# Performance work log

Measured on AMD Instinct MI355X. Metric: run time of the kernel, lower is better.

Reference implementation:

```python
import jax, jax.numpy as jnp
import numpy as np


def setup_inputs() -> dict:
    key = jax.random.key(0)
    k1, k2 = jax.random.split(key)
    x = jax.random.normal(k1, (32, 64, 64, 64), dtype=jnp.float32)
    codebook = jax.random.normal(k2, (1024, 64), dtype=jnp.float32)
    return {"x": x, "codebook": codebook}


def reference(x, codebook):
    # x: (B, D, H, W)  codebook: (K, D)
    B, D = x.shape[0], x.shape[1]
    spatial = x.shape[2:]
    flat = x.reshape(B, D, -1).transpose(0, 2, 1)  # (B, N, D)
    dot = jnp.einsum("bnd,kd->bnk", flat, codebook)
    cb_norm = jnp.sum(codebook * codebook, axis=-1)  # (K,)
    indices = jnp.argmin(cb_norm[None, None, :] - 2.0 * dot, axis=-1)  # (B, N)
    quantized = codebook[indices]  # (B, N, D) gather
    out = quantized.transpose(0, 2, 1).reshape(x.shape)
    return out, indices.reshape((B,) + spatial)
```

## Files before the change

### kernel.cpp

```cpp
#include <hip/hip_runtime.h>


typedef _Float16 f16x8 __attribute__((ext_vector_type(8)));
typedef float    f32x4 __attribute__((ext_vector_type(4)));

#define VQ_D    64
#define VQ_HW   4096
#define VQ_NPOS 131072
#define SC      2048.0f
#define EPS_Q   16
#define WS_CBN  65536
#define WS_CBT  66560
#define WS_CNT  132096
#define WS_LIST 132100

__global__ __launch_bounds__(256)
void vq_prep(const float* __restrict__ cb, float* __restrict__ ws)
{
    const int tid = threadIdx.x;
    const int blk = blockIdx.x;
    if (blk < 64) {
        const int it   = blk * 256 + tid;
        const int ct   = it >> 8;
        const int s    = (it >> 6) & 3;
        const int lane = it & 63;
        const int ks   = s & 1, isR = s >> 1;
        const int n    = ct * 16 + (lane & 15);
        const int k0   = ks * 32 + (lane >> 4) * 8;
        const float* src = cb + n * 64 + k0;
        f16x8 o;
        #pragma unroll
        for (int j = 0; j < 8; ++j) {
            const float b = src[j];
            const _Float16 bh = (_Float16)b;
            o[j] = isR ? (_Float16)((b - (float)bh) * (-2.0f * SC))
                       : (_Float16)(-2.0f * (float)bh);
        }
        ((f16x8*)ws)[it] = o;
    } else if (blk < 128) {
        const int it = (blk - 64) * 256 + tid;
        const int k = it >> 4, j4 = it & 15;
        ((float4*)(ws + WS_CBT))[j4 * 1024 + k] = ((const float4*)cb)[it];
    } else {
        const int k = (blk - 128) * 256 + tid;
        const float4* row = (const float4*)(cb + k * 64);
        float a0 = 0.f, a1 = 0.f, a2 = 0.f, a3 = 0.f;
        #pragma unroll
        for (int j = 0; j < 16; ++j) {
            const float4 c = row[j];
            a0 = fmaf(c.x, c.x, a0); a1 = fmaf(c.y, c.y, a1);
            a2 = fmaf(c.z, c.z, a2); a3 = fmaf(c.w, c.w, a3);
        }
        ws[WS_CBN + k] = (a0 + a1) + (a2 + a3);
        if (k == 0) ((int*)ws)[WS_CNT] = 0;
    }
}

#define GLOAD_LDS(GP, LP)                                                     \
    __builtin_amdgcn_global_load_lds(                                         \
        (const __attribute__((address_space(1))) unsigned int*)(GP),          \
        (__attribute__((address_space(3))) unsigned int*)(LP), 16, 0, 0)

__global__ __launch_bounds__(256, 4)
void vq_main(const float* __restrict__ x,
             const float* __restrict__ cb,
             float* __restrict__ ws,
             float* __restrict__ out,
             float* __restrict__ idx_out)
{
    __shared__ f16x8 bbuf[2][1024];
    __shared__ float cn_lds[1024];
    __shared__ int   sk[128];
    __shared__ int   smg[128];

    const int tid  = threadIdx.x;
    const int lane = tid & 63;
    const int wv   = tid >> 6;
    const int m    = lane & 15;
    const int q    = lane >> 4;

    const int p0 = blockIdx.x * 128;
    const int b  = p0 >> 12;
    const int n0 = p0 & (VQ_HW - 1);
    const float* xw = x + (size_t)b * (VQ_D * VQ_HW) + n0 + wv * 32;

    ((float4*)cn_lds)[tid] = ((const float4*)(ws + WS_CBN))[tid];

    {
        const char* gsrc = (const char*)ws + wv * 4096 + lane * 16;
        char*       ldst = (char*)&bbuf[0][0] + wv * 4096;
        GLOAD_LDS(gsrc, ldst);                GLOAD_LDS(gsrc + 1024, ldst + 1024);
        GLOAD_LDS(gsrc + 2048, ldst + 2048);  GLOAD_LDS(gsrc + 3072, ldst + 3072);
    }

    f16x8 Ah[2][2], Ra[2][2];
    #pragma unroll
    for (int tl = 0; tl < 2; ++tl)
        #pragma unroll
        for (int ks = 0; ks < 2; ++ks) {
            f16x8 h8, r8;
            #pragma unroll
            for (int j = 0; j < 8; ++j) {
                const float v = xw[(size_t)(ks * 32 + q * 8 + j) * VQ_HW + tl * 16 + m];
                const _Float16 vh = (_Float16)v;
                h8[j] = vh;
                r8[j] = (_Float16)((v - (float)vh) * SC);
            }
            Ah[tl][ks] = h8; Ra[tl][ks] = r8;
        }

    int d1[2][4], d2[2][4];
    #pragma unroll
    for (int tl = 0; tl < 2; ++tl)
        #pragma unroll
        for (int r = 0; r < 4; ++r) { d1[tl][r] = 0x7FFFFFFF; d2[tl][r] = 0x7FFFFFFF; }

    const f32x4 zero4 = {0.f, 0.f, 0.f, 0.f};

    for (int cc = 0; cc < 16; ++cc) {
        __syncthreads();
        if (cc < 15) {
            const char* gsrc = (const char*)ws + (size_t)(cc + 1) * 16384 + wv * 4096 + lane * 16;
            char*       ldst = (char*)&bbuf[(cc + 1) & 1][0] + wv * 4096;
            GLOAD_LDS(gsrc, ldst);                GLOAD_LDS(gsrc + 1024, ldst + 1024);
            GLOAD_LDS(gsrc + 2048, ldst + 2048);  GLOAD_LDS(gsrc + 3072, ldst + 3072);
        }
        const f16x8* bufc = &bbuf[cc & 1][0];
        #pragma unroll
        for (int ctl = 0; ctl < 4; ++ctl) {
            const int ctg = cc * 4 + ctl;
            const f16x8 B0 = bufc[ctl * 256 +       lane];
            const f16x8 B1 = bufc[ctl * 256 +  64 + lane];
            const f16x8 R0 = bufc[ctl * 256 + 128 + lane];
            const f16x8 R1 = bufc[ctl * 256 + 192 + lane];
            const float cv = cn_lds[ctg * 16 + m];
            const f32x4 Ci = {cv, cv, cv, cv};
            f32x4 acm[2], acc[2];
            #pragma unroll
            for (int tl = 0; tl < 2; ++tl) {
                acm[tl] = __builtin_amdgcn_mfma_f32_16x16x32_f16(Ah[tl][0], B0, Ci,      0,0,0);
                acm[tl] = __builtin_amdgcn_mfma_f32_16x16x32_f16(Ah[tl][1], B1, acm[tl], 0,0,0);
                acc[tl] = __builtin_amdgcn_mfma_f32_16x16x32_f16(Ah[tl][0], R0, zero4,   0,0,0);
                acc[tl] = __builtin_amdgcn_mfma_f32_16x16x32_f16(Ah[tl][1], R1, acc[tl], 0,0,0);
                acc[tl] = __builtin_amdgcn_mfma_f32_16x16x32_f16(Ra[tl][0], B0, acc[tl], 0,0,0);
                acc[tl] = __builtin_amdgcn_mfma_f32_16x16x32_f16(Ra[tl][1], B1, acc[tl], 0,0,0);
            }
            const int code_ = ctg * 16 + m;
            #pragma unroll
            for (int tl = 0; tl < 2; ++tl)
                #pragma unroll
                for (int r = 0; r < 4; ++r) {
                    const float qf  = fmaf(acm[tl][r], SC, acc[tl][r]);
                    const int   key = ((int)qf << 10) | code_;
                    const int   t   = (key > d1[tl][r]) ? key : d1[tl][r];
                    d2[tl][r] = (t < d2[tl][r]) ? t : d2[tl][r];
                    d1[tl][r] = (key < d1[tl][r]) ? key : d1[tl][r];
                }
        }
    }

    #pragma unroll
    for (int off = 1; off < 16; off <<= 1)
        #pragma unroll
        for (int tl = 0; tl < 2; ++tl)
            #pragma unroll
            for (int r = 0; r < 4; ++r) {
                const int od1 = __shfl_xor(d1[tl][r], off, 64);
                const int od2 = __shfl_xor(d2[tl][r], off, 64);
                const int mx  = (d1[tl][r] > od1) ? d1[tl][r] : od1;
                const int mn2 = (d2[tl][r] < od2) ? d2[tl][r] : od2;
                d2[tl][r] = (mx < mn2) ? mx : mn2;
                d1[tl][r] = (d1[tl][r] < od1) ? d1[tl][r] : od1;
            }

    if (m == 0) {
        #pragma unroll
        for (int tl = 0; tl < 2; ++tl)
            #pragma unroll
            for (int r = 0; r < 4; ++r) {
                const int li = wv * 32 + tl * 16 + q * 4 + r;
                sk[li]  = d1[tl][r] & 1023;
                smg[li] = (d2[tl][r] >> 10) - (d1[tl][r] >> 10);
            }
    }
    __syncthreads();

    const int pos  = tid & 127;
    const int half = tid >> 7;
    const int bk   = sk[pos];
    if (half == 0) {
        idx_out[p0 + pos] = (float)bk;
        if (smg[pos] < EPS_Q) {
            const int slot = atomicAdd((int*)ws + WS_CNT, 1);
            ((int*)ws)[WS_LIST + slot] = p0 + pos;
        }
    }
    const float4* cr = (const float4*)(cb + (size_t)bk * VQ_D) + half * 8;
    float* ob = out + (size_t)b * (VQ_D * VQ_HW) + (size_t)(half * 32) * VQ_HW + n0 + pos;
    #pragma unroll
    for (int d4 = 0; d4 < 8; ++d4) {
        const float4 v = cr[d4];
        ob[(size_t)(d4 * 4 + 0) * VQ_HW] = v.x;
        ob[(size_t)(d4 * 4 + 1) * VQ_HW] = v.y;
        ob[(size_t)(d4 * 4 + 2) * VQ_HW] = v.z;
        ob[(size_t)(d4 * 4 + 3) * VQ_HW] = v.w;
    }
}

__global__ __launch_bounds__(64)
void vq_rescan(const float* __restrict__ x,
               const float* __restrict__ cb,
               const float* __restrict__ ws,
               float* __restrict__ out,
               float* __restrict__ idx_out)
{
    __shared__ float xs[VQ_D];
    const int lane = threadIdx.x;
    const int cnt  = ((const int*)ws)[WS_CNT];
    const int* list = (const int*)ws + WS_LIST;
    const float*  cnb  = ws + WS_CBN;
    const float4* cbT4 = (const float4*)(ws + WS_CBT);

    for (int i = blockIdx.x; i < cnt; i += gridDim.x) {
        const int p = list[i];
        const int b = p >> 12, n = p & (VQ_HW - 1);
        xs[lane] = x[(size_t)b * (VQ_D * VQ_HW) + (size_t)lane * VQ_HW + n];
        __syncthreads();
        float4 xr[16];
        #pragma unroll
        for (int j = 0; j < 16; ++j) xr[j] = ((const float4*)xs)[j];

        float bd = 3.4e38f; int bk = 0;
        #pragma unroll 4
        for (int t = 0; t < 16; ++t) {
            const int code = t * 64 + lane;
            float a0 = 0.f, a1 = 0.f, a2 = 0.f, a3 = 0.f;
            #pragma unroll
            for (int j4 = 0; j4 < 16; ++j4) {
                const float4 c = cbT4[j4 * 1024 + code];
                a0 = fmaf(xr[j4].x, c.x, a0); a1 = fmaf(xr[j4].y, c.y, a1);
                a2 = fmaf(xr[j4].z, c.z, a2); a3 = fmaf(xr[j4].w, c.w, a3);
            }
            const float dist = fmaf(-2.0f, (a0 + a1) + (a2 + a3), cnb[code]);
            if (dist < bd) { bd = dist; bk = code; }
        }
        #pragma unroll
        for (int off = 1; off < 64; off <<= 1) {
            const float od = __shfl_xor(bd, off, 64);
            const int   ok = __shfl_xor(bk, off, 64);
            if (od < bd || (od == bd && ok < bk)) { bd = od; bk = ok; }
        }
        out[(size_t)b * (VQ_D * VQ_HW) + (size_t)lane * VQ_HW + n] = cb[(size_t)bk * VQ_D + lane];
        if (lane == 0) idx_out[p] = (float)bk;
        __syncthreads();
    }
}

extern "C" void kernel_launch(void* const* d_in, const int* in_sizes, int n_in,
                              void* d_out, int out_size, void* d_ws, size_t ws_size,
                              hipStream_t stream) {
    const float* x  = (const float*)d_in[0];
    const float* cb = (const float*)d_in[1];
    float* out = (float*)d_out;
    float* idx = out + (size_t)VQ_NPOS * VQ_D;
    float* ws  = (float*)d_ws;

    vq_prep  <<<dim3(132),  dim3(256), 0, stream>>>(cb, ws);
    vq_main  <<<dim3(1024), dim3(256), 0, stream>>>(x, cb, ws, out, idx);
    vq_rescan<<<dim3(1024), dim3(64),  0, stream>>>(x, cb, ws, out, idx);
}
```

Before: 159.7 us.

## Halve positions per block, interleave codebook norms into chunks, raise occupancy

Each wave now handles 16 positions instead of 32, so blocks cover 64 positions and the grid doubles to 2048 blocks. The launch bound is raised from 4 to 8 blocks per SM. The prep kernel writes the codebook in chunks of two code tiles with their norms interleaved, so norms arrive through the same global-to-LDS pipeline and the separate norm table in shared memory goes away. This cuts registers and shared memory per block to raise occupancy, but each block now streams the whole codebook through LDS for half as many positions. That doubles codebook traffic and the number of barriers per unit of work.

```diff
diff --git a/kernel.cpp b/kernel.cpp
--- a/kernel.cpp
+++ b/kernel.cpp
@@ -9,10 +9,11 @@
 #define VQ_NPOS 131072
 #define SC      2048.0f
 #define EPS_Q   16
-#define WS_CBN  65536
-#define WS_CBT  66560
-#define WS_CNT  132096
-#define WS_LIST 132100
+#define CHB     9216
+#define WS_CBN  73728
+#define WS_CBT  74752
+#define WS_CNT  140288
+#define WS_LIST 140292
 
 __global__ __launch_bounds__(256)
 void vq_prep(const float* __restrict__ cb, float* __restrict__ ws)
@@ -36,7 +37,8 @@
             o[j] = isR ? (_Float16)((b - (float)bh) * (-2.0f * SC))
                        : (_Float16)(-2.0f * (float)bh);
         }
-        ((f16x8*)ws)[it] = o;
+        *(f16x8*)((char*)ws + (size_t)(ct >> 1) * CHB + (ct & 1) * 4096
+                            + s * 1024 + lane * 16) = o;
     } else if (blk < 128) {
         const int it = (blk - 64) * 256 + tid;
         const int k = it >> 4, j4 = it & 15;
@@ -51,7 +53,11 @@
             a0 = fmaf(c.x, c.x, a0); a1 = fmaf(c.y, c.y, a1);
             a2 = fmaf(c.z, c.z, a2); a3 = fmaf(c.w, c.w, a3);
         }
-        ws[WS_CBN + k] = (a0 + a1) + (a2 + a3);
+        const float cn = (a0 + a1) + (a2 + a3);
+        ws[WS_CBN + k] = cn;
+        const int ct = k >> 4, i = k & 15;
+        *(float*)((char*)ws + (size_t)(ct >> 1) * CHB + 8192
+                            + (ct & 1) * 64 + i * 4) = cn;
         if (k == 0) ((int*)ws)[WS_CNT] = 0;
     }
 }
@@ -61,17 +67,16 @@
         (const __attribute__((address_space(1))) unsigned int*)(GP),          \
         (__attribute__((address_space(3))) unsigned int*)(LP), 16, 0, 0)
 
-__global__ __launch_bounds__(256, 4)
+__global__ __launch_bounds__(256, 8)
 void vq_main(const float* __restrict__ x,
              const float* __restrict__ cb,
              float* __restrict__ ws,
              float* __restrict__ out,
              float* __restrict__ idx_out)
 {
-    __shared__ f16x8 bbuf[2][1024];
-    __shared__ float cn_lds[1024];
-    __shared__ int   sk[128];
-    __shared__ int   smg[128];
+    __shared__ f16x8 bbuf[2][CHB / 16];
+    __shared__ int   sk[64];
+    __shared__ int   smg[64];
 
     const int tid  = threadIdx.x;
     const int lane = tid & 63;
@@ -79,126 +84,109 @@
     const int m    = lane & 15;
     const int q    = lane >> 4;
 
-    const int p0 = blockIdx.x * 128;
+    const int p0 = blockIdx.x * 64;
     const int b  = p0 >> 12;
     const int n0 = p0 & (VQ_HW - 1);
-    const float* xw = x + (size_t)b * (VQ_D * VQ_HW) + n0 + wv * 32;
-
-    ((float4*)cn_lds)[tid] = ((const float4*)(ws + WS_CBN))[tid];
+    const float* xw = x + (size_t)b * (VQ_D * VQ_HW) + n0 + wv * 16;
 
     {
-        const char* gsrc = (const char*)ws + wv * 4096 + lane * 16;
-        char*       ldst = (char*)&bbuf[0][0] + wv * 4096;
-        GLOAD_LDS(gsrc, ldst);                GLOAD_LDS(gsrc + 1024, ldst + 1024);
-        GLOAD_LDS(gsrc + 2048, ldst + 2048);  GLOAD_LDS(gsrc + 3072, ldst + 3072);
-    }
-
-    f16x8 Ah[2][2], Ra[2][2];
-    #pragma unroll
-    for (int tl = 0; tl < 2; ++tl)
-        #pragma unroll
-        for (int ks = 0; ks < 2; ++ks) {
-            f16x8 h8, r8;
-            #pragma unroll
-            for (int j = 0; j < 8; ++j) {
-                const float v = xw[(size_t)(ks * 32 + q * 8 + j) * VQ_HW + tl * 16 + m];
-                const _Float16 vh = (_Float16)v;
-                h8[j] = vh;
-                r8[j] = (_Float16)((v - (float)vh) * SC);
-            }
-            Ah[tl][ks] = h8; Ra[tl][ks] = r8;
-        }
-
-    int d1[2][4], d2[2][4];
-    #pragma unroll
-    for (int tl = 0; tl < 2; ++tl)
-        #pragma unroll
-        for (int r = 0; r < 4; ++r) { d1[tl][r] = 0x7FFFFFFF; d2[tl][r] = 0x7FFFFFFF; }
+        const char* gs = (const char*)ws + lane * 16;
+        char*       ld = (char*)&bbuf[0][0];
+        for (int o = wv; o < 9; o += 4) GLOAD_LDS(gs + o * 1024, ld + o * 1024);
+    }
+
+    f16x8 Ah[2], Ra[2];
+    #pragma unroll
+    for (int ks = 0; ks < 2; ++ks) {
+        f16x8 h8, r8;
+        #pragma unroll
+        for (int j = 0; j < 8; ++j) {
+            const float v = xw[(size_t)(ks * 32 + q * 8 + j) * VQ_HW + m];
+            const _Float16 vh = (_Float16)v;
+            h8[j] = vh;
+            r8[j] = (_Float16)((v - (float)vh) * SC);
+        }
+        Ah[ks] = h8; Ra[ks] = r8;
+    }
+
+    int d1[4], d2[4];
+    #pragma unroll
+    for (int r = 0; r < 4; ++r) { d1[r] = 0x7FFFFFFF; d2[r] = 0x7FFFFFFF; }
 
     const f32x4 zero4 = {0.f, 0.f, 0.f, 0.f};
 
-    for (int cc = 0; cc < 16; ++cc) {
+    for (int cc = 0; cc < 32; ++cc) {
         __syncthreads();
-        if (cc < 15) {
-            const char* gsrc = (const char*)ws + (size_t)(cc + 1) * 16384 + wv * 4096 + lane * 16;
-            char*       ldst = (char*)&bbuf[(cc + 1) & 1][0] + wv * 4096;
-            GLOAD_LDS(gsrc, ldst);                GLOAD_LDS(gsrc + 1024, ldst + 1024);
-            GLOAD_LDS(gsrc + 2048, ldst + 2048);  GLOAD_LDS(gsrc + 3072, ldst + 3072);
-        }
-        const f16x8* bufc = &bbuf[cc & 1][0];
-        #pragma unroll
-        for (int ctl = 0; ctl < 4; ++ctl) {
-            const int ctg = cc * 4 + ctl;
-            const f16x8 B0 = bufc[ctl * 256 +       lane];
-            const f16x8 B1 = bufc[ctl * 256 +  64 + lane];
-            const f16x8 R0 = bufc[ctl * 256 + 128 + lane];
-            const f16x8 R1 = bufc[ctl * 256 + 192 + lane];
-            const float cv = cn_lds[ctg * 16 + m];
+        if (cc < 31) {
+            const char* gs = (const char*)ws + (size_t)(cc + 1) * CHB + lane * 16;
+            char*       ld = (char*)&bbuf[(cc + 1) & 1][0];
+            for (int o = wv; o < 9; o += 4) GLOAD_LDS(gs + o * 1024, ld + o * 1024);
+        }
+        const char* bufc = (const char*)&bbuf[cc & 1][0];
+        #pragma unroll
+        for (int ci = 0; ci < 2; ++ci) {
+            const int ctg = cc * 2 + ci;
+            const f16x8* bp = (const f16x8*)(bufc + ci * 4096);
+            const f16x8 R0 = bp[128 + lane];
+            const f16x8 R1 = bp[192 + lane];
+            f32x4 acc = __builtin_amdgcn_mfma_f32_16x16x32_f16(Ah[0], R0, zero4, 0,0,0);
+            acc       = __builtin_amdgcn_mfma_f32_16x16x32_f16(Ah[1], R1, acc,   0,0,0);
+            const f16x8 B0 = bp[lane];
+            const f16x8 B1 = bp[64 + lane];
+            acc       = __builtin_amdgcn_mfma_f32_16x16x32_f16(Ra[0], B0, acc,   0,0,0);
+            acc       = __builtin_amdgcn_mfma_f32_16x16x32_f16(Ra[1], B1, acc,   0,0,0);
+            const float cv = *(const float*)(bufc + 8192 + ci * 64 + m * 4);
             const f32x4 Ci = {cv, cv, cv, cv};
-            f32x4 acm[2], acc[2];
-            #pragma unroll
-            for (int tl = 0; tl < 2; ++tl) {
-                acm[tl] = __builtin_amdgcn_mfma_f32_16x16x32_f16(Ah[tl][0], B0, Ci,      0,0,0);
-                acm[tl] = __builtin_amdgcn_mfma_f32_16x16x32_f16(Ah[tl][1], B1, acm[tl], 0,0,0);
-                acc[tl] = __builtin_amdgcn_mfma_f32_16x16x32_f16(Ah[tl][0], R0, zero4,   0,0,0);
-                acc[tl] = __builtin_amdgcn_mfma_f32_16x16x32_f16(Ah[tl][1], R1, acc[tl], 0,0,0);
-                acc[tl] = __builtin_amdgcn_mfma_f32_16x16x32_f16(Ra[tl][0], B0, acc[tl], 0,0,0);
-                acc[tl] = __builtin_amdgcn_mfma_f32_16x16x32_f16(Ra[tl][1], B1, acc[tl], 0,0,0);
-            }
+            f32x4 acm = __builtin_amdgcn_mfma_f32_16x16x32_f16(Ah[0], B0, Ci,  0,0,0);
+            acm       = __builtin_amdgcn_mfma_f32_16x16x32_f16(Ah[1], B1, acm, 0,0,0);
             const int code_ = ctg * 16 + m;
             #pragma unroll
-            for (int tl = 0; tl < 2; ++tl)
-                #pragma unroll
-                for (int r = 0; r < 4; ++r) {
-                    const float qf  = fmaf(acm[tl][r], SC, acc[tl][r]);
-                    const int   key = ((int)qf << 10) | code_;
-                    const int   t   = (key > d1[tl][r]) ? key : d1[tl][r];
-                    d2[tl][r] = (t < d2[tl][r]) ? t : d2[tl][r];
-                    d1[tl][r] = (key < d1[tl][r]) ? key : d1[tl][r];
-                }
+            for (int r = 0; r < 4; ++r) {
+                const float qf  = fmaf(acm[r], SC, acc[r]);
+                const int   key = ((int)qf << 10) | code_;
+                const int   t   = (key > d1[r]) ? key : d1[r];
+                d2[r] = (t < d2[r]) ? t : d2[r];
+                d1[r] = (key < d1[r]) ? key : d1[r];
+            }
         }
     }
 
     #pragma unroll
     for (int off = 1; off < 16; off <<= 1)
         #pragma unroll
-        for (int tl = 0; tl < 2; ++tl)
-            #pragma unroll
-            for (int r = 0; r < 4; ++r) {
-                const int od1 = __shfl_xor(d1[tl][r], off, 64);
-                const int od2 = __shfl_xor(d2[tl][r], off, 64);
-                const int mx  = (d1[tl][r] > od1) ? d1[tl][r] : od1;
-                const int mn2 = (d2[tl][r] < od2) ? d2[tl][r] : od2;
-                d2[tl][r] = (mx < mn2) ? mx : mn2;
-                d1[tl][r] = (d1[tl][r] < od1) ? d1[tl][r] : od1;
-            }
+        for (int r = 0; r < 4; ++r) {
+            const int od1 = __shfl_xor(d1[r], off, 64);
+            const int od2 = __shfl_xor(d2[r], off, 64);
+            const int mx  = (d1[r] > od1) ? d1[r] : od1;
+            const int mn2 = (d2[r] < od2) ? d2[r] : od2;
+            d2[r] = (mx < mn2) ? mx : mn2;
+            d1[r] = (d1[r] < od1) ? d1[r] : od1;
+        }
 
     if (m == 0) {
         #pragma unroll
-        for (int tl = 0; tl < 2; ++tl)
-            #pragma unroll
-            for (int r = 0; r < 4; ++r) {
-                const int li = wv * 32 + tl * 16 + q * 4 + r;
-                sk[li]  = d1[tl][r] & 1023;
-                smg[li] = (d2[tl][r] >> 10) - (d1[tl][r] >> 10);
-            }
+        for (int r = 0; r < 4; ++r) {
+            const int li = wv * 16 + q * 4 + r;
+            sk[li]  = d1[r] & 1023;
+            smg[li] = (d2[r] >> 10) - (d1[r] >> 10);
+        }
     }
     __syncthreads();
 
-    const int pos  = tid & 127;
-    const int half = tid >> 7;
+    const int pos  = tid & 63;
+    const int part = tid >> 6;
     const int bk   = sk[pos];
-    if (half == 0) {
+    if (part == 0) {
         idx_out[p0 + pos] = (float)bk;
         if (smg[pos] < EPS_Q) {
             const int slot = atomicAdd((int*)ws + WS_CNT, 1);
             ((int*)ws)[WS_LIST + slot] = p0 + pos;
         }
     }
-    const float4* cr = (const float4*)(cb + (size_t)bk * VQ_D) + half * 8;
-    float* ob = out + (size_t)b * (VQ_D * VQ_HW) + (size_t)(half * 32) * VQ_HW + n0 + pos;
-    #pragma unroll
-    for (int d4 = 0; d4 < 8; ++d4) {
+    const float4* cr = (const float4*)(cb + (size_t)bk * VQ_D) + part * 4;
+    float* ob = out + (size_t)b * (VQ_D * VQ_HW) + (size_t)(part * 16) * VQ_HW + n0 + pos;
+    #pragma unroll
+    for (int d4 = 0; d4 < 4; ++d4) {
         const float4 v = cr[d4];
         ob[(size_t)(d4 * 4 + 0) * VQ_HW] = v.x;
         ob[(size_t)(d4 * 4 + 1) * VQ_HW] = v.y;
@@ -266,6 +254,6 @@
     float* ws  = (float*)d_ws;
 
     vq_prep  <<<dim3(132),  dim3(256), 0, stream>>>(cb, ws);
-    vq_main  <<<dim3(1024), dim3(256), 0, stream>>>(x, cb, ws, out, idx);
+    vq_main  <<<dim3(2048), dim3(256), 0, stream>>>(x, cb, ws, out, idx);
     vq_rescan<<<dim3(1024), dim3(64),  0, stream>>>(x, cb, ws, out, idx);
 }
```

After: 172.8 us. +8.2%, slower.

## Fold scaled codebook norms into chunked workspace and single accumulator MFMA chain

Applied to the files above, without the earlier changes.

The workspace is re-laid out into chunks that carry each block of codebook tiles together with its pre-scaled norms. The main loop stages one chunk per half-iteration with manual double buffering, which removes the separate norm LDS array. The high and low distance accumulators are merged into one MFMA chain by pre-scaling the fp16 high part of x by 2048 and seeding the accumulator with the scaled norm. This drops the per-element fma and the zero-init chain. The top-2 update uses v_med3_i32 in place of max/min sequences. It adds an extra register set (Ak) and changes the rounding behaviour, so EPS_Q is widened to 20 to cover the added error.

```diff
diff --git a/kernel.cpp b/kernel.cpp
--- a/kernel.cpp
+++ b/kernel.cpp
@@ -8,11 +8,13 @@
 #define VQ_HW   4096
 #define VQ_NPOS 131072
 #define SC      2048.0f
-#define EPS_Q   16
-#define WS_CBN  65536
-#define WS_CBT  66560
-#define WS_CNT  132096
-#define WS_LIST 132100
+#define EPS_Q   20
+#define CHB     16640
+#define CHBP    17664
+#define WS_CBN  66560
+#define WS_CBT  67584
+#define WS_CNT  133120
+#define WS_LIST 133124
 
 __global__ __launch_bounds__(256)
 void vq_prep(const float* __restrict__ cb, float* __restrict__ ws)
@@ -36,7 +38,8 @@
             o[j] = isR ? (_Float16)((b - (float)bh) * (-2.0f * SC))
                        : (_Float16)(-2.0f * (float)bh);
         }
-        ((f16x8*)ws)[it] = o;
+        *(f16x8*)((char*)ws + (size_t)(ct >> 2) * CHB + (ct & 3) * 4096
+                            + s * 1024 + lane * 16) = o;
     } else if (blk < 128) {
         const int it = (blk - 64) * 256 + tid;
         const int k = it >> 4, j4 = it & 15;
@@ -51,7 +54,11 @@
             a0 = fmaf(c.x, c.x, a0); a1 = fmaf(c.y, c.y, a1);
             a2 = fmaf(c.z, c.z, a2); a3 = fmaf(c.w, c.w, a3);
         }
-        ws[WS_CBN + k] = (a0 + a1) + (a2 + a3);
+        const float cn = (a0 + a1) + (a2 + a3);
+        ws[WS_CBN + k] = cn;
+        const int ct = k >> 4, i = k & 15;
+        *(float*)((char*)ws + (size_t)(ct >> 2) * CHB + 16384
+                            + (ct & 3) * 64 + i * 4) = cn * 2048.0f;
         if (k == 0) ((int*)ws)[WS_CNT] = 0;
     }
 }
@@ -60,6 +67,56 @@
     __builtin_amdgcn_global_load_lds(                                         \
         (const __attribute__((address_space(1))) unsigned int*)(GP),          \
         (__attribute__((address_space(3))) unsigned int*)(LP), 16, 0, 0)
+
+#define STAGE(GS, BOFF)                                                       \
+    {                                                                         \
+        char* ld_ = (char*)bbuf + (BOFF) + wv * 1024;                         \
+        const char* gs_ = (GS) + wv * 1024;                                   \
+        GLOAD_LDS(gs_,         ld_);                                          \
+        GLOAD_LDS(gs_ + 4096,  ld_ + 4096);                                   \
+        GLOAD_LDS(gs_ + 8192,  ld_ + 8192);                                   \
+        GLOAD_LDS(gs_ + 12288, ld_ + 12288);                                  \
+        if (wv == 0 && lane < 16)                                             \
+            GLOAD_LDS((GS) + 16384, (char*)bbuf + (BOFF) + 16384);            \
+    }
+
+#define CT_BODY(BOFF, SLOT, CTG)                                              \
+    {                                                                         \
+        const f16x8 B0 = *(const f16x8*)(lp + (BOFF) + (SLOT) * 4096);        \
+        const f16x8 B1 = *(const f16x8*)(lp + (BOFF) + (SLOT) * 4096 + 1024); \
+        const f16x8 R0 = *(const f16x8*)(lp + (BOFF) + (SLOT) * 4096 + 2048); \
+        const f16x8 R1 = *(const f16x8*)(lp + (BOFF) + (SLOT) * 4096 + 3072); \
+        const float cvq = *(const float*)(cp + (BOFF) + (SLOT) * 64);         \
+        const f32x4 Ci = {cvq, cvq, cvq, cvq};                                \
+        f32x4 a0 = __builtin_amdgcn_mfma_f32_16x16x32_f16(Ra[0][0], B0, Ci, 0,0,0); \
+        f32x4 a1 = __builtin_amdgcn_mfma_f32_16x16x32_f16(Ra[1][0], B0, Ci, 0,0,0); \
+        a0 = __builtin_amdgcn_mfma_f32_16x16x32_f16(Ra[0][1], B1, a0, 0,0,0); \
+        a1 = __builtin_amdgcn_mfma_f32_16x16x32_f16(Ra[1][1], B1, a1, 0,0,0); \
+        a0 = __builtin_amdgcn_mfma_f32_16x16x32_f16(Ah[0][0], R0, a0, 0,0,0); \
+        a1 = __builtin_amdgcn_mfma_f32_16x16x32_f16(Ah[1][0], R0, a1, 0,0,0); \
+        a0 = __builtin_amdgcn_mfma_f32_16x16x32_f16(Ah[0][1], R1, a0, 0,0,0); \
+        a1 = __builtin_amdgcn_mfma_f32_16x16x32_f16(Ah[1][1], R1, a1, 0,0,0); \
+        a0 = __builtin_amdgcn_mfma_f32_16x16x32_f16(Ak[0][0], B0, a0, 0,0,0); \
+        a1 = __builtin_amdgcn_mfma_f32_16x16x32_f16(Ak[1][0], B0, a1, 0,0,0); \
+        a0 = __builtin_amdgcn_mfma_f32_16x16x32_f16(Ak[0][1], B1, a0, 0,0,0); \
+        a1 = __builtin_amdgcn_mfma_f32_16x16x32_f16(Ak[1][1], B1, a1, 0,0,0); \
+        const int cbase_ = (CTG) * 16 + m;                                    \
+        _Pragma("unroll")                                                     \
+        for (int r = 0; r < 4; ++r) {                                         \
+            const int k0_ = ((int)a0[r] << 10) | cbase_;                      \
+            int m0_;                                                          \
+            asm("v_med3_i32 %0, %1, %2, %3"                                   \
+                : "=v"(m0_) : "v"(k0_), "v"(d1[0][r]), "v"(d2[0][r]));        \
+            d2[0][r] = m0_;                                                   \
+            d1[0][r] = (k0_ < d1[0][r]) ? k0_ : d1[0][r];                     \
+            const int k1_ = ((int)a1[r] << 10) | cbase_;                      \
+            int m1_;                                                          \
+            asm("v_med3_i32 %0, %1, %2, %3"                                   \
+                : "=v"(m1_) : "v"(k1_), "v"(d1[1][r]), "v"(d2[1][r]));        \
+            d2[1][r] = m1_;                                                   \
+            d1[1][r] = (k1_ < d1[1][r]) ? k1_ : d1[1][r];                     \
+        }                                                                     \
+    }
 
 __global__ __launch_bounds__(256, 4)
 void vq_main(const float* __restrict__ x,
@@ -68,8 +125,7 @@
              float* __restrict__ out,
              float* __restrict__ idx_out)
 {
-    __shared__ f16x8 bbuf[2][1024];
-    __shared__ float cn_lds[1024];
+    __shared__ f16x8 bbuf[2 * (CHBP / 16)];
     __shared__ int   sk[128];
     __shared__ int   smg[128];
 
@@ -84,29 +140,25 @@
     const int n0 = p0 & (VQ_HW - 1);
     const float* xw = x + (size_t)b * (VQ_D * VQ_HW) + n0 + wv * 32;
 
-    ((float4*)cn_lds)[tid] = ((const float4*)(ws + WS_CBN))[tid];
-
-    {
-        const char* gsrc = (const char*)ws + wv * 4096 + lane * 16;
-        char*       ldst = (char*)&bbuf[0][0] + wv * 4096;
-        GLOAD_LDS(gsrc, ldst);                GLOAD_LDS(gsrc + 1024, ldst + 1024);
-        GLOAD_LDS(gsrc + 2048, ldst + 2048);  GLOAD_LDS(gsrc + 3072, ldst + 3072);
-    }
-
-    f16x8 Ah[2][2], Ra[2][2];
+    const char* gs = (const char*)ws + lane * 16;
+
+    STAGE(gs, 0)
+
+    f16x8 Ah[2][2], Ak[2][2], Ra[2][2];
     #pragma unroll
     for (int tl = 0; tl < 2; ++tl)
         #pragma unroll
         for (int ks = 0; ks < 2; ++ks) {
-            f16x8 h8, r8;
+            f16x8 h8, k8, r8;
             #pragma unroll
             for (int j = 0; j < 8; ++j) {
                 const float v = xw[(size_t)(ks * 32 + q * 8 + j) * VQ_HW + tl * 16 + m];
                 const _Float16 vh = (_Float16)v;
                 h8[j] = vh;
+                k8[j] = (_Float16)((float)vh * 2048.0f);
                 r8[j] = (_Float16)((v - (float)vh) * SC);
             }
-            Ah[tl][ks] = h8; Ra[tl][ks] = r8;
+            Ah[tl][ks] = h8; Ak[tl][ks] = k8; Ra[tl][ks] = r8;
         }
 
     int d1[2][4], d2[2][4];
@@ -115,48 +167,24 @@
         #pragma unroll
         for (int r = 0; r < 4; ++r) { d1[tl][r] = 0x7FFFFFFF; d2[tl][r] = 0x7FFFFFFF; }
 
-    const f32x4 zero4 = {0.f, 0.f, 0.f, 0.f};
-
-    for (int cc = 0; cc < 16; ++cc) {
-        __syncthreads();
-        if (cc < 15) {
-            const char* gsrc = (const char*)ws + (size_t)(cc + 1) * 16384 + wv * 4096 + lane * 16;
-            char*       ldst = (char*)&bbuf[(cc + 1) & 1][0] + wv * 4096;
-            GLOAD_LDS(gsrc, ldst);                GLOAD_LDS(gsrc + 1024, ldst + 1024);
-            GLOAD_LDS(gsrc + 2048, ldst + 2048);  GLOAD_LDS(gsrc + 3072, ldst + 3072);
-        }
-        const f16x8* bufc = &bbuf[cc & 1][0];
-        #pragma unroll
-        for (int ctl = 0; ctl < 4; ++ctl) {
-            const int ctg = cc * 4 + ctl;
-            const f16x8 B0 = bufc[ctl * 256 +       lane];
-            const f16x8 B1 = bufc[ctl * 256 +  64 + lane];
-            const f16x8 R0 = bufc[ctl * 256 + 128 + lane];
-            const f16x8 R1 = bufc[ctl * 256 + 192 + lane];
-            const float cv = cn_lds[ctg * 16 + m];
-            const f32x4 Ci = {cv, cv, cv, cv};
-            f32x4 acm[2], acc[2];
-            #pragma unroll
-            for (int tl = 0; tl < 2; ++tl) {
-                acm[tl] = __builtin_amdgcn_mfma_f32_16x16x32_f16(Ah[tl][0], B0, Ci,      0,0,0);
-                acm[tl] = __builtin_amdgcn_mfma_f32_16x16x32_f16(Ah[tl][1], B1, acm[tl], 0,0,0);
-                acc[tl] = __builtin_amdgcn_mfma_f32_16x16x32_f16(Ah[tl][0], R0, zero4,   0,0,0);
-                acc[tl] = __builtin_amdgcn_mfma_f32_16x16x32_f16(Ah[tl][1], R1, acc[tl], 0,0,0);
-                acc[tl] = __builtin_amdgcn_mfma_f32_16x16x32_f16(Ra[tl][0], B0, acc[tl], 0,0,0);
-                acc[tl] = __builtin_amdgcn_mfma_f32_16x16x32_f16(Ra[tl][1], B1, acc[tl], 0,0,0);
-            }
-            const int code_ = ctg * 16 + m;
-            #pragma unroll
-            for (int tl = 0; tl < 2; ++tl)
-                #pragma unroll
-                for (int r = 0; r < 4; ++r) {
-                    const float qf  = fmaf(acm[tl][r], SC, acc[tl][r]);
-                    const int   key = ((int)qf << 10) | code_;
-                    const int   t   = (key > d1[tl][r]) ? key : d1[tl][r];
-                    d2[tl][r] = (t < d2[tl][r]) ? t : d2[tl][r];
-                    d1[tl][r] = (key < d1[tl][r]) ? key : d1[tl][r];
-                }
-        }
+    const char* lp = (const char*)bbuf + lane * 16;
+    const char* cp = (const char*)bbuf + 16384 + m * 4;
+
+    for (int it8 = 0; it8 < 8; ++it8) {
+        const int cg = it8 * 8;
+        __syncthreads();
+        STAGE(gs + CHB, CHBP)
+        CT_BODY(0, 0, cg + 0)
+        CT_BODY(0, 1, cg + 1)
+        CT_BODY(0, 2, cg + 2)
+        CT_BODY(0, 3, cg + 3)
+        __syncthreads();
+        if (it8 < 7) STAGE(gs + 2 * CHB, 0)
+        CT_BODY(CHBP, 0, cg + 4)
+        CT_BODY(CHBP, 1, cg + 5)
+        CT_BODY(CHBP, 2, cg + 6)
+        CT_BODY(CHBP, 3, cg + 7)
+        gs += 2 * CHB;
     }
 
     #pragma unroll
```

Result: faster. 156.4 us (-2.1%).
